# Kernel tuning notes

Hardware: AMD Instinct MI355X
Metric: run time of the kernel (lower is better)

## Reference

```python
import jax, jax.numpy as jnp
import numpy as np

N_NODES = 100000
N_EDGES = 600000
VOCAB = 5000
NUM_GRAPHS = 2000
NUM_CLASSES = 10


def setup_inputs() -> dict:
    key = jax.random.key(0)
    ks = jax.random.split(key, 12)
    x = jax.random.randint(ks[0], (N_NODES,), 0, VOCAB, dtype=jnp.int32)
    edge_index = jax.random.randint(ks[1], (2, N_EDGES), 0, N_NODES, dtype=jnp.int32)
    batch = jnp.sort(jax.random.randint(ks[2], (N_NODES,), 0, NUM_GRAPHS, dtype=jnp.int32))
    emb = jax.random.normal(ks[3], (VOCAB, 64), dtype=jnp.float32) * 0.1
    W1 = jax.random.normal(ks[4], (64, 128), dtype=jnp.float32) * (1.0 / np.sqrt(64))
    b1 = jnp.zeros((128,), dtype=jnp.float32)
    W2 = jax.random.normal(ks[5], (128, 128), dtype=jnp.float32) * (1.0 / np.sqrt(128))
    b2 = jnp.zeros((128,), dtype=jnp.float32)
    Wlin = jax.random.normal(ks[6], (128, NUM_CLASSES), dtype=jnp.float32) * (1.0 / np.sqrt(128))
    blin = jnp.zeros((NUM_CLASSES,), dtype=jnp.float32)
    return {"x": x, "edge_index": edge_index, "batch": batch, "num_graphs": NUM_GRAPHS,
            "emb": emb, "W1": W1, "b1": b1, "W2": W2, "b2": b2, "Wlin": Wlin, "blin": blin}


def reference(x, edge_index, batch, num_graphs, emb, W1, b1, W2, b2, Wlin, blin):
    N = x.shape[0]
    loops = jnp.arange(N, dtype=edge_index.dtype)
    src = jnp.concatenate([edge_index[0], loops])  # message sources (j)
    dst = jnp.concatenate([edge_index[1], loops])  # aggregation targets (i)
    # GCN symmetric normalization with self-loops (PyG gcn_norm, source_to_target)
    deg = jax.ops.segment_sum(jnp.ones_like(dst, dtype=jnp.float32), dst, num_segments=N)
    dinv = jnp.where(deg > 0, jax.lax.rsqrt(deg), 0.0)
    norm = dinv[src] * dinv[dst]  # [E+N]

    def gcn(h, W, b):
        h = h @ W  # linear transform first (GCNConv order)
        msg = h[src] * norm[:, None]  # gather + scale, [E+N, F]
        return jax.ops.segment_sum(msg, dst, num_segments=N) + b

    h = emb[x]  # [N, 64]
    h = jax.nn.relu(gcn(h, W1, b1))
    h = jax.nn.relu(gcn(h, W2, b2))
    g = jax.ops.segment_max(h, batch, num_segments=num_graphs)  # global_max_pool
    return g @ Wlin + blin
```

## Files before the change

kernel.cpp:

```cpp
#include <hip/hip_runtime.h>
#include <hip/hip_bf16.h>
#include <hip/hip_fp16.h>


typedef _Float16 h8 __attribute__((ext_vector_type(8)));
typedef _Float16 h4v __attribute__((ext_vector_type(4)));
typedef float f32x4 __attribute__((ext_vector_type(4)));

__global__ __launch_bounds__(256) void k_zero(int4* __restrict__ deg, int n4i,
                                              int4* __restrict__ pool, int p4i) {
    int t = blockIdx.x * 256 + threadIdx.x;
    int4 z = make_int4(0, 0, 0, 0);
    if (t < n4i) deg[t] = z;
    if (t < p4i) pool[t] = z;
}

__global__ __launch_bounds__(256) void k_degprep(const int* __restrict__ dst, int* __restrict__ deg, int E,
                                                 const float* __restrict__ emb, __half2* __restrict__ e16,
                                                 const float* __restrict__ W1, _Float16* __restrict__ W1T,
                                                 const float* __restrict__ W2, _Float16* __restrict__ W2T,
                                                 int nEmbF, int gE, int nCast) {
    int bid = blockIdx.x;
    if (bid < gE) {
        int e = bid * 256 + threadIdx.x;
        if (e < E) atomicAdd(&deg[dst[e]], 1);
    } else if (bid < gE + nCast) {
        int t = (bid - gE) * 256 + threadIdx.x;
        if (t * 4 < nEmbF) {
            float4 v = *(const float4*)&emb[t * 4];
            e16[t * 2] = __floats2half2_rn(v.x, v.y);
            e16[t * 2 + 1] = __floats2half2_rn(v.z, v.w);
        }
    } else if (bid < gE + nCast + 32) {
        int t = (bid - gE - nCast) * 256 + threadIdx.x;
        int c = t >> 6, k = t & 63;
        W1T[c * 64 + k] = (_Float16)W1[k * 128 + c];
    } else {
        int t = (bid - gE - nCast - 32) * 256 + threadIdx.x;
        if (t < 128 * 128) {
            int c = t >> 7, k = t & 127;
            W2T[c * 128 + k] = (_Float16)W2[k * 128 + c];
        }
    }
}

__global__ __launch_bounds__(256) void k_scan1(const int* __restrict__ deg, int* __restrict__ exc,
                                               int* __restrict__ bsums, float* __restrict__ dinv, int N) {
    __shared__ int s[256];
    int i = blockIdx.x * 256 + threadIdx.x;
    int v = (i < N) ? deg[i] : 0;
    if (i < N) dinv[i] = rsqrtf((float)(v + 1));
    s[threadIdx.x] = v;
    __syncthreads();
    for (int off = 1; off < 256; off <<= 1) {
        int t = (threadIdx.x >= (unsigned)off) ? s[threadIdx.x - off] : 0;
        __syncthreads();
        s[threadIdx.x] += t;
        __syncthreads();
    }
    if (i < N) exc[i] = s[threadIdx.x] - v;
    if (threadIdx.x == 255) bsums[blockIdx.x] = s[255];
}

__global__ __launch_bounds__(512) void k_scan2(int* __restrict__ bsums, int nb) {
    __shared__ int s[512];
    int i = threadIdx.x;
    int v = (i < nb) ? bsums[i] : 0;
    s[i] = v;
    __syncthreads();
    for (int off = 1; off < 512; off <<= 1) {
        int t = (i >= off) ? s[i - off] : 0;
        __syncthreads();
        s[i] += t;
        __syncthreads();
    }
    if (i < nb) bsums[i] = s[i] - v;
}

__global__ __launch_bounds__(256) void k_scan3(int* __restrict__ rowstart, int* __restrict__ cursor,
                                               const int* __restrict__ bsums, int N, int E) {
    int i = blockIdx.x * 256 + threadIdx.x;
    if (i < N) {
        int r = rowstart[i] + bsums[blockIdx.x];
        rowstart[i] = r;
        cursor[i] = r;
    }
    if (i == 0 && blockIdx.x == 0) rowstart[N] = E;
}

__global__ __launch_bounds__(256) void k_fill(const int* __restrict__ src, const int* __restrict__ dst,
                                              const int* __restrict__ x, const float* __restrict__ dinv,
                                              int* __restrict__ cursor, int2* __restrict__ ed,
                                              int* __restrict__ cols, int E) {
    int e = blockIdx.x * 256 + threadIdx.x;
    if (e < E) {
        int d = dst[e];
        int s = src[e];
        int pos = atomicAdd(&cursor[d], 1);
        ed[pos] = make_int2(x[s], __float_as_int(dinv[s]));
        cols[pos] = s;
    }
}

__global__ __launch_bounds__(512) void k_mlp(const __half2* __restrict__ e16, const int* __restrict__ x,
                                             const float* __restrict__ dinv, const int* __restrict__ rs,
                                             const int2* __restrict__ ed, const _Float16* __restrict__ W1T,
                                             const float* __restrict__ b1, const _Float16* __restrict__ W2T,
                                             _Float16* __restrict__ P, int N) {
    __shared__ _Float16 Xs[64][72];
    __shared__ _Float16 Hs[64][136];
    int tid = threadIdx.x;
    int blk0 = blockIdx.x * 64;
    {
        int lane = tid & 31;
        int hw = tid >> 5;
        int p = lane >> 3;
        int f16 = lane & 7;
        const h8* e8 = (const h8*)e16;
#pragma unroll
        for (int pass = 0; pass < 2; ++pass) {
            int nlA = hw * 4 + pass * 2, nlB = nlA + 1;
            int gA = blk0 + nlA; if (gA >= N) gA = N - 1;
            int gB = blk0 + nlB; if (gB >= N) gB = N - 1;
            int cA0 = rs[gA], cA1 = rs[gA + 1];
            int cB0 = rs[gB], cB1 = rs[gB + 1];
            int baseA = (cA0 < cA1) ? cA1 - 1 : 0;
            int baseB = (cB0 < cB1) ? cB1 - 1 : 0;
            float dA = dinv[gA], dB = dinv[gB];
            h8 selfA = e8[(size_t)x[gA] * 8 + f16];
            h8 selfB = e8[(size_t)x[gB] * 8 + f16];
            float accA[8] = {}, accB[8] = {};
            {
                int eA0 = cA0 + p, eA1 = cA0 + 4 + p;
                int eB0 = cB0 + p, eB1 = cB0 + 4 + p;
                int2 rA0 = ed[(eA0 < cA1) ? eA0 : baseA];
                int2 rA1 = ed[(eA1 < cA1) ? eA1 : baseA];
                int2 rB0 = ed[(eB0 < cB1) ? eB0 : baseB];
                int2 rB1 = ed[(eB1 < cB1) ? eB1 : baseB];
                h8 tA0 = e8[(size_t)rA0.x * 8 + f16];
                h8 tA1 = e8[(size_t)rA1.x * 8 + f16];
                h8 tB0 = e8[(size_t)rB0.x * 8 + f16];
                h8 tB1 = e8[(size_t)rB1.x * 8 + f16];
                float wA0 = (eA0 < cA1) ? __int_as_float(rA0.y) : 0.f;
                float wA1 = (eA1 < cA1) ? __int_as_float(rA1.y) : 0.f;
                float wB0 = (eB0 < cB1) ? __int_as_float(rB0.y) : 0.f;
                float wB1 = (eB1 < cB1) ? __int_as_float(rB1.y) : 0.f;
#pragma unroll
                for (int f = 0; f < 8; ++f) {
                    accA[f] = fmaf(wA1, (float)tA1[f], fmaf(wA0, (float)tA0[f], accA[f]));
                    accB[f] = fmaf(wB1, (float)tB1[f], fmaf(wB0, (float)tB0[f], accB[f]));
                }
            }
            for (int eb = cA0 + 8; eb < cA1; eb += 8) {
                int e0 = eb + p, e1i = eb + 4 + p;
                int2 r0 = ed[(e0 < cA1) ? e0 : cA1 - 1];
                int2 r1 = ed[(e1i < cA1) ? e1i : cA1 - 1];
                h8 t0 = e8[(size_t)r0.x * 8 + f16];
                h8 t1 = e8[(size_t)r1.x * 8 + f16];
                float w0 = (e0 < cA1) ? __int_as_float(r0.y) : 0.f;
                float w1 = (e1i < cA1) ? __int_as_float(r1.y) : 0.f;
#pragma unroll
                for (int f = 0; f < 8; ++f)
                    accA[f] = fmaf(w1, (float)t1[f], fmaf(w0, (float)t0[f], accA[f]));
            }
            for (int eb = cB0 + 8; eb < cB1; eb += 8) {
                int e0 = eb + p, e1i = eb + 4 + p;
                int2 r0 = ed[(e0 < cB1) ? e0 : cB1 - 1];
                int2 r1 = ed[(e1i < cB1) ? e1i : cB1 - 1];
                h8 t0 = e8[(size_t)r0.x * 8 + f16];
                h8 t1 = e8[(size_t)r1.x * 8 + f16];
                float w0 = (e0 < cB1) ? __int_as_float(r0.y) : 0.f;
                float w1 = (e1i < cB1) ? __int_as_float(r1.y) : 0.f;
#pragma unroll
                for (int f = 0; f < 8; ++f)
                    accB[f] = fmaf(w1, (float)t1[f], fmaf(w0, (float)t0[f], accB[f]));
            }
            h8 yA, yB;
#pragma unroll
            for (int f = 0; f < 8; ++f) {
                float a = accA[f];
                a += __shfl_xor(a, 8);
                a += __shfl_xor(a, 16);
                float b = accB[f];
                b += __shfl_xor(b, 8);
                b += __shfl_xor(b, 16);
                yA[f] = (_Float16)(dA * fmaf(dA, (float)selfA[f], a));
                yB[f] = (_Float16)(dB * fmaf(dB, (float)selfB[f], b));
            }
            if (p == 0) {
                *(h8*)&Xs[nlA][f16 * 8] = yA;
                *(h8*)&Xs[nlB][f16 * 8] = yB;
            }
        }
    }
    __syncthreads();
    int l = tid & 63, wid = tid >> 6;
    int r = l & 15, kg = l >> 4;
    int rb = wid & 3;
    int ch = wid >> 2;
    {
        f32x4 acc[4];
#pragma unroll
        for (int ct = 0; ct < 4; ++ct) acc[ct] = (f32x4){0.f, 0.f, 0.f, 0.f};
#pragma unroll
        for (int kc = 0; kc < 2; ++kc) {
            h8 a = *(const h8*)&Xs[rb * 16 + r][kc * 32 + kg * 8];
#pragma unroll
            for (int ct = 0; ct < 4; ++ct) {
                h8 b = *(const h8*)(W1T + (size_t)(ch * 64 + ct * 16 + r) * 64 + kc * 32 + kg * 8);
                acc[ct] = __builtin_amdgcn_mfma_f32_16x16x32_f16(a, b, acc[ct], 0, 0, 0);
            }
        }
#pragma unroll
        for (int ct = 0; ct < 4; ++ct) {
            float bias = b1[ch * 64 + ct * 16 + r];
#pragma unroll
            for (int i = 0; i < 4; ++i)
                Hs[rb * 16 + 4 * kg + i][ch * 64 + ct * 16 + r] =
                    (_Float16)fmaxf(acc[ct][i] + bias, 0.f);
        }
    }
    __syncthreads();
    {
        f32x4 acc[4];
#pragma unroll
        for (int ct = 0; ct < 4; ++ct) acc[ct] = (f32x4){0.f, 0.f, 0.f, 0.f};
#pragma unroll
        for (int kc = 0; kc < 4; ++kc) {
            h8 a = *(const h8*)&Hs[rb * 16 + r][kc * 32 + kg * 8];
#pragma unroll
            for (int ct = 0; ct < 4; ++ct) {
                h8 b = *(const h8*)(W2T + (size_t)(ch * 64 + ct * 16 + r) * 128 + kc * 32 + kg * 8);
                acc[ct] = __builtin_amdgcn_mfma_f32_16x16x32_f16(a, b, acc[ct], 0, 0, 0);
            }
        }
        float dv[4];
#pragma unroll
        for (int i = 0; i < 4; ++i) {
            int gr = blk0 + rb * 16 + 4 * kg + i;
            dv[i] = (gr < N) ? dinv[gr] : 0.f;
        }
#pragma unroll
        for (int ct = 0; ct < 4; ++ct) {
#pragma unroll
            for (int i = 0; i < 4; ++i) {
                int gr = blk0 + rb * 16 + 4 * kg + i;
                if (gr < N)
                    P[(size_t)gr * 128 + ch * 64 + ct * 16 + r] = (_Float16)(acc[ct][i] * dv[i]);
            }
        }
    }
}

__global__ __launch_bounds__(256) void k_agg2pool(const h4v* __restrict__ P4, const int* __restrict__ batch,
                                                  const float* __restrict__ dinv, const int* __restrict__ rs,
                                                  const int* __restrict__ cols, const float4* __restrict__ bias4,
                                                  float* __restrict__ pool, int N, int G) {
    __shared__ int lpool[4][128];
    int tid = threadIdx.x;
    lpool[tid >> 7][tid & 127] = 0;
    lpool[(tid >> 7) + 2][tid & 127] = 0;
    __syncthreads();
    int lane = tid & 31;
    int blk_n0 = blockIdx.x * 16;
    int gfirst = batch[(blk_n0 < N) ? blk_n0 : (N - 1)];
    int n0 = blk_n0 + (tid >> 5) * 2;
    if (n0 < N) {
        int nA = n0;
        int nB = (n0 + 1 < N) ? n0 + 1 : n0;
        int cA0 = rs[nA], cA1 = rs[nA + 1];
        int cB0 = rs[nB], cB1 = rs[nB + 1];
        bool hasA = cA0 < cA1, hasB = cB0 < cB1;
        h4v sA = P4[(size_t)nA * 32 + lane];
        h4v sB = P4[(size_t)nB * 32 + lane];
        float aA[4], aB[4];
#pragma unroll
        for (int f = 0; f < 4; ++f) {
            aA[f] = (float)sA[f];
            aB[f] = (float)sB[f];
        }
        {
            h4v tA[16], tB[16];
#pragma unroll
            for (int i = 0; i < 16; ++i) {
                int ei = cA0 + i;
                int ec = (ei < cA1) ? ei : (hasA ? cA1 - 1 : 0);
                tA[i] = P4[(size_t)cols[ec] * 32 + lane];
            }
#pragma unroll
            for (int i = 0; i < 16; ++i) {
                int ei = cB0 + i;
                int ec = (ei < cB1) ? ei : (hasB ? cB1 - 1 : 0);
                tB[i] = P4[(size_t)cols[ec] * 32 + lane];
            }
#pragma unroll
            for (int i = 0; i < 16; ++i) {
                float w = (cA0 + i < cA1) ? 1.f : 0.f;
#pragma unroll
                for (int f = 0; f < 4; ++f) aA[f] = fmaf(w, (float)tA[i][f], aA[f]);
            }
#pragma unroll
            for (int i = 0; i < 16; ++i) {
                float w = (cB0 + i < cB1) ? 1.f : 0.f;
#pragma unroll
                for (int f = 0; f < 4; ++f) aB[f] = fmaf(w, (float)tB[i][f], aB[f]);
            }
        }
        for (int e = cA0 + 16; e < cA1; e += 16) {
            h4v t[16];
#pragma unroll
            for (int i = 0; i < 16; ++i) {
                int ei = e + i;
                int ec = (ei < cA1) ? ei : cA1 - 1;
                t[i] = P4[(size_t)cols[ec] * 32 + lane];
            }
#pragma unroll
            for (int i = 0; i < 16; ++i) {
                float w = (e + i < cA1) ? 1.f : 0.f;
#pragma unroll
                for (int f = 0; f < 4; ++f) aA[f] = fmaf(w, (float)t[i][f], aA[f]);
            }
        }
        for (int e = cB0 + 16; e < cB1; e += 16) {
            h4v t[16];
#pragma unroll
            for (int i = 0; i < 16; ++i) {
                int ei = e + i;
                int ec = (ei < cB1) ? ei : cB1 - 1;
                t[i] = P4[(size_t)cols[ec] * 32 + lane];
            }
#pragma unroll
            for (int i = 0; i < 16; ++i) {
                float w = (e + i < cB1) ? 1.f : 0.f;
#pragma unroll
                for (int f = 0; f < 4; ++f) aB[f] = fmaf(w, (float)t[i][f], aB[f]);
            }
        }
        float dA = dinv[nA], dB = dinv[nB];
        int gA = batch[nA], gB = batch[nB];
        float4 b = bias4[lane];
        float bv[4] = {b.x, b.y, b.z, b.w};
        float zA[4], zB[4];
#pragma unroll
        for (int f = 0; f < 4; ++f) {
            zA[f] = fmaxf(fmaf(dA, aA[f], bv[f]), 0.f);
            zB[f] = fmaxf(fmaf(dB, aB[f], bv[f]), 0.f);
        }
        int rot = (lane >> 3) & 3;
        auto emit = [&](int g, const float* m) {
            int slot = g - gfirst;
            if (slot < 4) {
#pragma unroll
                for (int f = 0; f < 4; ++f) {
                    int ff = (f + rot) & 3;
                    if (m[ff] > 0.f) atomicMax(&lpool[slot][lane * 4 + ff], __float_as_int(m[ff]));
                }
            } else {
                float* pg = pool + (size_t)g * 128 + lane * 4;
#pragma unroll
                for (int f = 0; f < 4; ++f)
                    if (m[f] > 0.f) atomicMax((int*)(pg + f), __float_as_int(m[f]));
            }
        };
        if (gA == gB) {
            float m[4];
#pragma unroll
            for (int f = 0; f < 4; ++f) m[f] = fmaxf(zA[f], zB[f]);
            emit(gA, m);
        } else {
            emit(gA, zA);
            emit(gB, zB);
        }
    }
    __syncthreads();
    {
        int f = tid & 127;
        for (int s = tid >> 7; s < 4; s += 2) {
            int v = lpool[s][f];
            if (v > 0) atomicMax((int*)&pool[(size_t)(gfirst + s) * 128 + f], v);
        }
    }
}

__global__ __launch_bounds__(256) void k_final(const float* __restrict__ pool, const float* __restrict__ Wlin,
                                               const float* __restrict__ blin, float* __restrict__ out, int G) {
    int t = blockIdx.x * 256 + threadIdx.x;
    if (t >= G * 10) return;
    int g = t / 10, c = t % 10;
    float acc = blin[c];
    const float* pr = pool + (size_t)g * 128;
#pragma unroll 8
    for (int f = 0; f < 128; ++f) acc = fmaf(pr[f], Wlin[f * 10 + c], acc);
    out[t] = acc;
}

extern "C" void kernel_launch(void* const* d_in, const int* in_sizes, int n_in,
                              void* d_out, int out_size, void* d_ws, size_t ws_size,
                              hipStream_t stream) {
    const int* x = (const int*)d_in[0];
    const int* ei = (const int*)d_in[1];
    const int* batch = (const int*)d_in[2];
    const float* emb = (const float*)d_in[4];
    const float* W1 = (const float*)d_in[5];
    const float* b1 = (const float*)d_in[6];
    const float* W2 = (const float*)d_in[7];
    const float* b2 = (const float*)d_in[8];
    const float* Wlin = (const float*)d_in[9];
    const float* blin = (const float*)d_in[10];
    float* out = (float*)d_out;

    int N = in_sizes[0];
    int E = in_sizes[1] / 2;
    int VOCAB = in_sizes[4] / 64;
    int G = out_size / 10;
    const int* srcp = ei;
    const int* dstp = ei + E;

    char* p = (char*)d_ws;
    auto alloc = [&](size_t bytes) -> char* {
        char* r = p;
        p += (bytes + 255) & ~(size_t)255;
        return r;
    };
    int* deg = (int*)alloc((size_t)N * 4);
    int* cursor = (int*)alloc((size_t)N * 4);
    int* rowstart = (int*)alloc((size_t)(N + 1) * 4);
    int* bsums = (int*)alloc(512 * 4);
    float* dinv = (float*)alloc((size_t)N * 4);
    int2* ed = (int2*)alloc((size_t)E * 8);
    int* cols = (int*)alloc((size_t)E * 4);
    _Float16* e16 = (_Float16*)alloc((size_t)VOCAB * 64 * 2);
    _Float16* W1T = (_Float16*)alloc(128 * 64 * 2);
    _Float16* W2T = (_Float16*)alloc(128 * 128 * 2);
    _Float16* P = (_Float16*)alloc((size_t)N * 128 * 2);
    float* pool = (float*)alloc((size_t)G * 128 * 4);

    int gE = (E + 255) / 256;
    int gN = (N + 255) / 256;
    int nEmbF = VOCAB * 64;
    int nCast = (nEmbF / 4 + 255) / 256;

    int n4i = N / 4, p4i = G * 128 / 4;
    int zg = ((n4i > p4i ? n4i : p4i) + 255) / 256;
    k_zero<<<zg, 256, 0, stream>>>((int4*)deg, n4i, (int4*)pool, p4i);
    k_degprep<<<gE + nCast + 32 + 64, 256, 0, stream>>>(dstp, deg, E, emb, (__half2*)e16, W1, W1T,
                                                        W2, W2T, nEmbF, gE, nCast);
    k_scan1<<<gN, 256, 0, stream>>>(deg, rowstart, bsums, dinv, N);
    k_scan2<<<1, 512, 0, stream>>>(bsums, gN);
    k_scan3<<<gN, 256, 0, stream>>>(rowstart, cursor, bsums, N, E);
    k_fill<<<gE, 256, 0, stream>>>(srcp, dstp, x, dinv, cursor, ed, cols, E);
    k_mlp<<<(N + 63) / 64, 512, 0, stream>>>((const __half2*)e16, x, dinv, rowstart, ed, W1T, b1,
                                             W2T, P, N);
    k_agg2pool<<<(N + 15) / 16, 256, 0, stream>>>((const h4v*)P, batch, dinv, rowstart, cols,
                                                  (const float4*)b2, pool, N, G);
    k_final<<<(G * 10 + 255) / 256, 256, 0, stream>>>(pool, Wlin, blin, out, G);
}
```

Measured before the change: 185.8 us.

## Halve MLP tile rows and split agg2pool edges across half-warps with 8-wide loads

k_mlp now processes 32 nodes per block instead of 64. Each half-warp handles one pair of nodes in a single pass, and each wave computes two 16-column MFMA tiles instead of four, which doubles the block count and shortens the per-block critical path. k_agg2pool now uses 16 lanes with 8-half loads per node row and splits the edges between two half-warps, combining them with a shuffle, so fewer, wider gathers are issued per edge. Only one half-warp emits the pooling atomics. The trade-off is more blocks and W1/W2 reloads in the MLP, plus an extra shuffle reduction in the aggregation.

```diff
diff --git a/kernel.cpp b/kernel.cpp
--- a/kernel.cpp
+++ b/kernel.cpp
@@ -4,7 +4,6 @@
 
 
 typedef _Float16 h8 __attribute__((ext_vector_type(8)));
-typedef _Float16 h4v __attribute__((ext_vector_type(4)));
 typedef float f32x4 __attribute__((ext_vector_type(4)));
 
 __global__ __launch_bounds__(256) void k_zero(int4* __restrict__ deg, int n4i,
@@ -107,130 +106,127 @@
                                              const int2* __restrict__ ed, const _Float16* __restrict__ W1T,
                                              const float* __restrict__ b1, const _Float16* __restrict__ W2T,
                                              _Float16* __restrict__ P, int N) {
-    __shared__ _Float16 Xs[64][72];
-    __shared__ _Float16 Hs[64][136];
+    __shared__ _Float16 Xs[32][72];
+    __shared__ _Float16 Hs[32][136];
     int tid = threadIdx.x;
-    int blk0 = blockIdx.x * 64;
+    int blk0 = blockIdx.x * 32;
     {
         int lane = tid & 31;
         int hw = tid >> 5;
         int p = lane >> 3;
         int f16 = lane & 7;
         const h8* e8 = (const h8*)e16;
-#pragma unroll
-        for (int pass = 0; pass < 2; ++pass) {
-            int nlA = hw * 4 + pass * 2, nlB = nlA + 1;
-            int gA = blk0 + nlA; if (gA >= N) gA = N - 1;
-            int gB = blk0 + nlB; if (gB >= N) gB = N - 1;
-            int cA0 = rs[gA], cA1 = rs[gA + 1];
-            int cB0 = rs[gB], cB1 = rs[gB + 1];
-            int baseA = (cA0 < cA1) ? cA1 - 1 : 0;
-            int baseB = (cB0 < cB1) ? cB1 - 1 : 0;
-            float dA = dinv[gA], dB = dinv[gB];
-            h8 selfA = e8[(size_t)x[gA] * 8 + f16];
-            h8 selfB = e8[(size_t)x[gB] * 8 + f16];
-            float accA[8] = {}, accB[8] = {};
-            {
-                int eA0 = cA0 + p, eA1 = cA0 + 4 + p;
-                int eB0 = cB0 + p, eB1 = cB0 + 4 + p;
-                int2 rA0 = ed[(eA0 < cA1) ? eA0 : baseA];
-                int2 rA1 = ed[(eA1 < cA1) ? eA1 : baseA];
-                int2 rB0 = ed[(eB0 < cB1) ? eB0 : baseB];
-                int2 rB1 = ed[(eB1 < cB1) ? eB1 : baseB];
-                h8 tA0 = e8[(size_t)rA0.x * 8 + f16];
-                h8 tA1 = e8[(size_t)rA1.x * 8 + f16];
-                h8 tB0 = e8[(size_t)rB0.x * 8 + f16];
-                h8 tB1 = e8[(size_t)rB1.x * 8 + f16];
-                float wA0 = (eA0 < cA1) ? __int_as_float(rA0.y) : 0.f;
-                float wA1 = (eA1 < cA1) ? __int_as_float(rA1.y) : 0.f;
-                float wB0 = (eB0 < cB1) ? __int_as_float(rB0.y) : 0.f;
-                float wB1 = (eB1 < cB1) ? __int_as_float(rB1.y) : 0.f;
-#pragma unroll
-                for (int f = 0; f < 8; ++f) {
-                    accA[f] = fmaf(wA1, (float)tA1[f], fmaf(wA0, (float)tA0[f], accA[f]));
-                    accB[f] = fmaf(wB1, (float)tB1[f], fmaf(wB0, (float)tB0[f], accB[f]));
-                }
-            }
-            for (int eb = cA0 + 8; eb < cA1; eb += 8) {
-                int e0 = eb + p, e1i = eb + 4 + p;
-                int2 r0 = ed[(e0 < cA1) ? e0 : cA1 - 1];
-                int2 r1 = ed[(e1i < cA1) ? e1i : cA1 - 1];
-                h8 t0 = e8[(size_t)r0.x * 8 + f16];
-                h8 t1 = e8[(size_t)r1.x * 8 + f16];
-                float w0 = (e0 < cA1) ? __int_as_float(r0.y) : 0.f;
-                float w1 = (e1i < cA1) ? __int_as_float(r1.y) : 0.f;
-#pragma unroll
-                for (int f = 0; f < 8; ++f)
-                    accA[f] = fmaf(w1, (float)t1[f], fmaf(w0, (float)t0[f], accA[f]));
-            }
-            for (int eb = cB0 + 8; eb < cB1; eb += 8) {
-                int e0 = eb + p, e1i = eb + 4 + p;
-                int2 r0 = ed[(e0 < cB1) ? e0 : cB1 - 1];
-                int2 r1 = ed[(e1i < cB1) ? e1i : cB1 - 1];
-                h8 t0 = e8[(size_t)r0.x * 8 + f16];
-                h8 t1 = e8[(size_t)r1.x * 8 + f16];
-                float w0 = (e0 < cB1) ? __int_as_float(r0.y) : 0.f;
-                float w1 = (e1i < cB1) ? __int_as_float(r1.y) : 0.f;
-#pragma unroll
-                for (int f = 0; f < 8; ++f)
-                    accB[f] = fmaf(w1, (float)t1[f], fmaf(w0, (float)t0[f], accB[f]));
-            }
-            h8 yA, yB;
+        int nlA = hw * 2, nlB = nlA + 1;
+        int gA = blk0 + nlA; if (gA >= N) gA = N - 1;
+        int gB = blk0 + nlB; if (gB >= N) gB = N - 1;
+        int cA0 = rs[gA], cA1 = rs[gA + 1];
+        int cB0 = rs[gB], cB1 = rs[gB + 1];
+        int baseA = (cA0 < cA1) ? cA1 - 1 : 0;
+        int baseB = (cB0 < cB1) ? cB1 - 1 : 0;
+        float dA = dinv[gA], dB = dinv[gB];
+        h8 selfA = e8[(size_t)x[gA] * 8 + f16];
+        h8 selfB = e8[(size_t)x[gB] * 8 + f16];
+        float accA[8] = {}, accB[8] = {};
+        {
+            int eA0 = cA0 + p, eA1 = cA0 + 4 + p;
+            int eB0 = cB0 + p, eB1 = cB0 + 4 + p;
+            int2 rA0 = ed[(eA0 < cA1) ? eA0 : baseA];
+            int2 rA1 = ed[(eA1 < cA1) ? eA1 : baseA];
+            int2 rB0 = ed[(eB0 < cB1) ? eB0 : baseB];
+            int2 rB1 = ed[(eB1 < cB1) ? eB1 : baseB];
+            h8 tA0 = e8[(size_t)rA0.x * 8 + f16];
+            h8 tA1 = e8[(size_t)rA1.x * 8 + f16];
+            h8 tB0 = e8[(size_t)rB0.x * 8 + f16];
+            h8 tB1 = e8[(size_t)rB1.x * 8 + f16];
+            float wA0 = (eA0 < cA1) ? __int_as_float(rA0.y) : 0.f;
+            float wA1 = (eA1 < cA1) ? __int_as_float(rA1.y) : 0.f;
+            float wB0 = (eB0 < cB1) ? __int_as_float(rB0.y) : 0.f;
+            float wB1 = (eB1 < cB1) ? __int_as_float(rB1.y) : 0.f;
 #pragma unroll
             for (int f = 0; f < 8; ++f) {
-                float a = accA[f];
-                a += __shfl_xor(a, 8);
-                a += __shfl_xor(a, 16);
-                float b = accB[f];
-                b += __shfl_xor(b, 8);
-                b += __shfl_xor(b, 16);
-                yA[f] = (_Float16)(dA * fmaf(dA, (float)selfA[f], a));
-                yB[f] = (_Float16)(dB * fmaf(dB, (float)selfB[f], b));
-            }
-            if (p == 0) {
-                *(h8*)&Xs[nlA][f16 * 8] = yA;
-                *(h8*)&Xs[nlB][f16 * 8] = yB;
-            }
+                accA[f] = fmaf(wA1, (float)tA1[f], fmaf(wA0, (float)tA0[f], accA[f]));
+                accB[f] = fmaf(wB1, (float)tB1[f], fmaf(wB0, (float)tB0[f], accB[f]));
+            }
+        }
+        for (int eb = cA0 + 8; eb < cA1; eb += 8) {
+            int e0 = eb + p, e1i = eb + 4 + p;
+            int2 r0 = ed[(e0 < cA1) ? e0 : cA1 - 1];
+            int2 r1 = ed[(e1i < cA1) ? e1i : cA1 - 1];
+            h8 t0 = e8[(size_t)r0.x * 8 + f16];
+            h8 t1 = e8[(size_t)r1.x * 8 + f16];
+            float w0 = (e0 < cA1) ? __int_as_float(r0.y) : 0.f;
+            float w1 = (e1i < cA1) ? __int_as_float(r1.y) : 0.f;
+#pragma unroll
+            for (int f = 0; f < 8; ++f)
+                accA[f] = fmaf(w1, (float)t1[f], fmaf(w0, (float)t0[f], accA[f]));
+        }
+        for (int eb = cB0 + 8; eb < cB1; eb += 8) {
+            int e0 = eb + p, e1i = eb + 4 + p;
+            int2 r0 = ed[(e0 < cB1) ? e0 : cB1 - 1];
+            int2 r1 = ed[(e1i < cB1) ? e1i : cB1 - 1];
+            h8 t0 = e8[(size_t)r0.x * 8 + f16];
+            h8 t1 = e8[(size_t)r1.x * 8 + f16];
+            float w0 = (e0 < cB1) ? __int_as_float(r0.y) : 0.f;
+            float w1 = (e1i < cB1) ? __int_as_float(r1.y) : 0.f;
+#pragma unroll
+            for (int f = 0; f < 8; ++f)
+                accB[f] = fmaf(w1, (float)t1[f], fmaf(w0, (float)t0[f], accB[f]));
+        }
+        h8 yA, yB;
+#pragma unroll
+        for (int f = 0; f < 8; ++f) {
+            float a = accA[f];
+            a += __shfl_xor(a, 8);
+            a += __shfl_xor(a, 16);
+            float b = accB[f];
+            b += __shfl_xor(b, 8);
+            b += __shfl_xor(b, 16);
+            yA[f] = (_Float16)(dA * fmaf(dA, (float)selfA[f], a));
+            yB[f] = (_Float16)(dB * fmaf(dB, (float)selfB[f], b));
+        }
+        if (p == 0) {
+            *(h8*)&Xs[nlA][f16 * 8] = yA;
+            *(h8*)&Xs[nlB][f16 * 8] = yB;
         }
     }
     __syncthreads();
     int l = tid & 63, wid = tid >> 6;
     int r = l & 15, kg = l >> 4;
-    int rb = wid & 3;
-    int ch = wid >> 2;
+    int rb = wid & 1;
+    int ch = wid >> 1;
     {
-        f32x4 acc[4];
-#pragma unroll
-        for (int ct = 0; ct < 4; ++ct) acc[ct] = (f32x4){0.f, 0.f, 0.f, 0.f};
+        f32x4 acc[2];
+#pragma unroll
+        for (int ct = 0; ct < 2; ++ct) acc[ct] = (f32x4){0.f, 0.f, 0.f, 0.f};
 #pragma unroll
         for (int kc = 0; kc < 2; ++kc) {
             h8 a = *(const h8*)&Xs[rb * 16 + r][kc * 32 + kg * 8];
 #pragma unroll
-            for (int ct = 0; ct < 4; ++ct) {
-                h8 b = *(const h8*)(W1T + (size_t)(ch * 64 + ct * 16 + r) * 64 + kc * 32 + kg * 8);
+            for (int ct = 0; ct < 2; ++ct) {
+                h8 b = *(const h8*)(W1T + (size_t)(ch * 32 + ct * 16 + r) * 64 + kc * 32 + kg * 8);
                 acc[ct] = __builtin_amdgcn_mfma_f32_16x16x32_f16(a, b, acc[ct], 0, 0, 0);
             }
         }
 #pragma unroll
-        for (int ct = 0; ct < 4; ++ct) {
-            float bias = b1[ch * 64 + ct * 16 + r];
+        for (int ct = 0; ct < 2; ++ct) {
+            float bias = b1[ch * 32 + ct * 16 + r];
 #pragma unroll
             for (int i = 0; i < 4; ++i)
-                Hs[rb * 16 + 4 * kg + i][ch * 64 + ct * 16 + r] =
+                Hs[rb * 16 + 4 * kg + i][ch * 32 + ct * 16 + r] =
                     (_Float16)fmaxf(acc[ct][i] + bias, 0.f);
         }
     }
     __syncthreads();
     {
-        f32x4 acc[4];
-#pragma unroll
-        for (int ct = 0; ct < 4; ++ct) acc[ct] = (f32x4){0.f, 0.f, 0.f, 0.f};
+        f32x4 acc[2];
+#pragma unroll
+        for (int ct = 0; ct < 2; ++ct) acc[ct] = (f32x4){0.f, 0.f, 0.f, 0.f};
 #pragma unroll
         for (int kc = 0; kc < 4; ++kc) {
             h8 a = *(const h8*)&Hs[rb * 16 + r][kc * 32 + kg * 8];
 #pragma unroll
-            for (int ct = 0; ct < 4; ++ct) {
-                h8 b = *(const h8*)(W2T + (size_t)(ch * 64 + ct * 16 + r) * 128 + kc * 32 + kg * 8);
+            for (int ct = 0; ct < 2; ++ct) {
+                h8 b = *(const h8*)(W2T + (size_t)(ch * 32 + ct * 16 + r) * 128 + kc * 32 + kg * 8);
                 acc[ct] = __builtin_amdgcn_mfma_f32_16x16x32_f16(a, b, acc[ct], 0, 0, 0);
             }
         }
@@ -241,20 +237,20 @@
             dv[i] = (gr < N) ? dinv[gr] : 0.f;
         }
 #pragma unroll
-        for (int ct = 0; ct < 4; ++ct) {
+        for (int ct = 0; ct < 2; ++ct) {
 #pragma unroll
             for (int i = 0; i < 4; ++i) {
                 int gr = blk0 + rb * 16 + 4 * kg + i;
                 if (gr < N)
-                    P[(size_t)gr * 128 + ch * 64 + ct * 16 + r] = (_Float16)(acc[ct][i] * dv[i]);
-            }
-        }
-    }
-}
-
-__global__ __launch_bounds__(256) void k_agg2pool(const h4v* __restrict__ P4, const int* __restrict__ batch,
+                    P[(size_t)gr * 128 + ch * 32 + ct * 16 + r] = (_Float16)(acc[ct][i] * dv[i]);
+            }
+        }
+    }
+}
+
+__global__ __launch_bounds__(256) void k_agg2pool(const h8* __restrict__ P8, const int* __restrict__ batch,
                                                   const float* __restrict__ dinv, const int* __restrict__ rs,
-                                                  const int* __restrict__ cols, const float4* __restrict__ bias4,
+                                                  const int* __restrict__ cols, const float* __restrict__ b2,
                                                   float* __restrict__ pool, int N, int G) {
     __shared__ int lpool[4][128];
     int tid = threadIdx.x;
@@ -262,6 +258,8 @@
     lpool[(tid >> 7) + 2][tid & 127] = 0;
     __syncthreads();
     int lane = tid & 31;
+    int p = lane >> 4;
+    int s = lane & 15;
     int blk_n0 = blockIdx.x * 16;
     int gfirst = batch[(blk_n0 < N) ? blk_n0 : (N - 1)];
     int n0 = blk_n0 + (tid >> 5) * 2;
@@ -271,101 +269,98 @@
         int cA0 = rs[nA], cA1 = rs[nA + 1];
         int cB0 = rs[nB], cB1 = rs[nB + 1];
         bool hasA = cA0 < cA1, hasB = cB0 < cB1;
-        h4v sA = P4[(size_t)nA * 32 + lane];
-        h4v sB = P4[(size_t)nB * 32 + lane];
-        float aA[4], aB[4];
-#pragma unroll
-        for (int f = 0; f < 4; ++f) {
-            aA[f] = (float)sA[f];
-            aB[f] = (float)sB[f];
-        }
+        h8 sA = P8[(size_t)nA * 16 + s];
+        h8 sB = P8[(size_t)nB * 16 + s];
+        float aA[8] = {}, aB[8] = {};
         {
-            h4v tA[16], tB[16];
-#pragma unroll
-            for (int i = 0; i < 16; ++i) {
-                int ei = cA0 + i;
+            h8 tA[8], tB[8];
+            float wA[8], wB[8];
+#pragma unroll
+            for (int i = 0; i < 8; ++i) {
+                int ei = cA0 + 2 * i + p;
                 int ec = (ei < cA1) ? ei : (hasA ? cA1 - 1 : 0);
-                tA[i] = P4[(size_t)cols[ec] * 32 + lane];
-            }
-#pragma unroll
-            for (int i = 0; i < 16; ++i) {
-                int ei = cB0 + i;
+                tA[i] = P8[(size_t)cols[ec] * 16 + s];
+                wA[i] = (ei < cA1) ? 1.f : 0.f;
+            }
+#pragma unroll
+            for (int i = 0; i < 8; ++i) {
+                int ei = cB0 + 2 * i + p;
                 int ec = (ei < cB1) ? ei : (hasB ? cB1 - 1 : 0);
-                tB[i] = P4[(size_t)cols[ec] * 32 + lane];
-            }
-#pragma unroll
-            for (int i = 0; i < 16; ++i) {
-                float w = (cA0 + i < cA1) ? 1.f : 0.f;
-#pragma unroll
-                for (int f = 0; f < 4; ++f) aA[f] = fmaf(w, (float)tA[i][f], aA[f]);
-            }
-#pragma unroll
-            for (int i = 0; i < 16; ++i) {
-                float w = (cB0 + i < cB1) ? 1.f : 0.f;
-#pragma unroll
-                for (int f = 0; f < 4; ++f) aB[f] = fmaf(w, (float)tB[i][f], aB[f]);
-            }
-        }
-        for (int e = cA0 + 16; e < cA1; e += 16) {
-            h4v t[16];
-#pragma unroll
-            for (int i = 0; i < 16; ++i) {
-                int ei = e + i;
+                tB[i] = P8[(size_t)cols[ec] * 16 + s];
+                wB[i] = (ei < cB1) ? 1.f : 0.f;
+            }
+#pragma unroll
+            for (int i = 0; i < 8; ++i)
+#pragma unroll
+                for (int f = 0; f < 8; ++f) aA[f] = fmaf(wA[i], (float)tA[i][f], aA[f]);
+#pragma unroll
+            for (int i = 0; i < 8; ++i)
+#pragma unroll
+                for (int f = 0; f < 8; ++f) aB[f] = fmaf(wB[i], (float)tB[i][f], aB[f]);
+        }
+        for (int eb = cA0 + 16; eb < cA1; eb += 16) {
+            h8 t[8];
+            float w[8];
+#pragma unroll
+            for (int i = 0; i < 8; ++i) {
+                int ei = eb + 2 * i + p;
                 int ec = (ei < cA1) ? ei : cA1 - 1;
-                t[i] = P4[(size_t)cols[ec] * 32 + lane];
-            }
-#pragma unroll
-            for (int i = 0; i < 16; ++i) {
-                float w = (e + i < cA1) ? 1.f : 0.f;
-#pragma unroll
-                for (int f = 0; f < 4; ++f) aA[f] = fmaf(w, (float)t[i][f], aA[f]);
-            }
-        }
-        for (int e = cB0 + 16; e < cB1; e += 16) {
-            h4v t[16];
-#pragma unroll
-            for (int i = 0; i < 16; ++i) {
-                int ei = e + i;
+                t[i] = P8[(size_t)cols[ec] * 16 + s];
+                w[i] = (ei < cA1) ? 1.f : 0.f;
+            }
+#pragma unroll
+            for (int i = 0; i < 8; ++i)
+#pragma unroll
+                for (int f = 0; f < 8; ++f) aA[f] = fmaf(w[i], (float)t[i][f], aA[f]);
+        }
+        for (int eb = cB0 + 16; eb < cB1; eb += 16) {
+            h8 t[8];
+            float w[8];
+#pragma unroll
+            for (int i = 0; i < 8; ++i) {
+                int ei = eb + 2 * i + p;
                 int ec = (ei < cB1) ? ei : cB1 - 1;
-                t[i] = P4[(size_t)cols[ec] * 32 + lane];
-            }
-#pragma unroll
-            for (int i = 0; i < 16; ++i) {
-                float w = (e + i < cB1) ? 1.f : 0.f;
-#pragma unroll
-                for (int f = 0; f < 4; ++f) aB[f] = fmaf(w, (float)t[i][f], aB[f]);
-            }
+                t[i] = P8[(size_t)cols[ec] * 16 + s];
+                w[i] = (ei < cB1) ? 1.f : 0.f;
+            }
+#pragma unroll
+            for (int i = 0; i < 8; ++i)
+#pragma unroll
+                for (int f = 0; f < 8; ++f) aB[f] = fmaf(w[i], (float)t[i][f], aB[f]);
         }
         float dA = dinv[nA], dB = dinv[nB];
         int gA = batch[nA], gB = batch[nB];
-        float4 b = bias4[lane];
-        float bv[4] = {b.x, b.y, b.z, b.w};
-        float zA[4], zB[4];
-#pragma unroll
-        for (int f = 0; f < 4; ++f) {
-            zA[f] = fmaxf(fmaf(dA, aA[f], bv[f]), 0.f);
-            zB[f] = fmaxf(fmaf(dB, aB[f], bv[f]), 0.f);
-        }
-        int rot = (lane >> 3) & 3;
+        float4 bb0 = *(const float4*)&b2[s * 8];
+        float4 bb1 = *(const float4*)&b2[s * 8 + 4];
+        float bv[8] = {bb0.x, bb0.y, bb0.z, bb0.w, bb1.x, bb1.y, bb1.z, bb1.w};
+        float zA[8], zB[8];
+#pragma unroll
+        for (int f = 0; f < 8; ++f) {
+            float a = aA[f] + __shfl_xor(aA[f], 16);
+            float b = aB[f] + __shfl_xor(aB[f], 16);
+            zA[f] = fmaxf(fmaf(dA, (float)sA[f] + a, bv[f]), 0.f);
+            zB[f] = fmaxf(fmaf(dB, (float)sB[f] + b, bv[f]), 0.f);
+        }
         auto emit = [&](int g, const float* m) {
+            if (p != 0) return;
             int slot = g - gfirst;
             if (slot < 4) {
 #pragma unroll
-                for (int f = 0; f < 4; ++f) {
-                    int ff = (f + rot) & 3;
-                    if (m[ff] > 0.f) atomicMax(&lpool[slot][lane * 4 + ff], __float_as_int(m[ff]));
+                for (int f = 0; f < 8; ++f) {
+                    int ff = (f + s) & 7;
+                    if (m[ff] > 0.f) atomicMax(&lpool[slot][s * 8 + ff], __float_as_int(m[ff]));
                 }
             } else {
-                float* pg = pool + (size_t)g * 128 + lane * 4;
-#pragma unroll
-                for (int f = 0; f < 4; ++f)
+                float* pg = pool + (size_t)g * 128 + s * 8;
+#pragma unroll
+                for (int f = 0; f < 8; ++f)
                     if (m[f] > 0.f) atomicMax((int*)(pg + f), __float_as_int(m[f]));
             }
         };
         if (gA == gB) {
-            float m[4];
-#pragma unroll
-            for (int f = 0; f < 4; ++f) m[f] = fmaxf(zA[f], zB[f]);
+            float m[8];
+#pragma unroll
+            for (int f = 0; f < 8; ++f) m[f] = fmaxf(zA[f], zB[f]);
             emit(gA, m);
         } else {
             emit(gA, zA);
@@ -375,9 +370,9 @@
     __syncthreads();
     {
         int f = tid & 127;
-        for (int s = tid >> 7; s < 4; s += 2) {
-            int v = lpool[s][f];
-            if (v > 0) atomicMax((int*)&pool[(size_t)(gfirst + s) * 128 + f], v);
+        for (int sl = tid >> 7; sl < 4; sl += 2) {
+            int v = lpool[sl][f];
+            if (v > 0) atomicMax((int*)&pool[(size_t)(gfirst + sl) * 128 + f], v);
         }
     }
 }
@@ -449,9 +444,9 @@
     k_scan2<<<1, 512, 0, stream>>>(bsums, gN);
     k_scan3<<<gN, 256, 0, stream>>>(rowstart, cursor, bsums, N, E);
     k_fill<<<gE, 256, 0, stream>>>(srcp, dstp, x, dinv, cursor, ed, cols, E);
-    k_mlp<<<(N + 63) / 64, 512, 0, stream>>>((const __half2*)e16, x, dinv, rowstart, ed, W1T, b1,
+    k_mlp<<<(N + 31) / 32, 512, 0, stream>>>((const __half2*)e16, x, dinv, rowstart, ed, W1T, b1,
                                              W2T, P, N);
-    k_agg2pool<<<(N + 15) / 16, 256, 0, stream>>>((const h4v*)P, batch, dinv, rowstart, cols,
-                                                  (const float4*)b2, pool, N, G);
+    k_agg2pool<<<(N + 15) / 16, 256, 0, stream>>>((const h8*)P, batch, dinv, rowstart, cols,
+                                                  b2, pool, N, G);
     k_final<<<(G * 10 + 255) / 256, 256, 0, stream>>>(pool, Wlin, blin, out, G);
 }
```

After: 180.3 us. 2.9% less time.
